# Kernel optimization log

Hardware: AMD Instinct MI355X
Metric: run time of the kernel (lower is better)

Reference implementation:

```python
import jax, jax.numpy as jnp
import numpy as np
from jax.ops import segment_sum, segment_max

N_NODES = 100000
N_EDGES = 1600000
IN_CH = 128
HIDDEN = 128
OUT_CH = 64
HEADS1 = 8


def _lin_params(key, din, dout, scale):
    kw, kb = jax.random.split(key)
    W = jax.random.normal(kw, (din, dout), jnp.float32) * scale
    b = jax.random.normal(kb, (dout,), jnp.float32) * 0.01
    return W, b


def setup_inputs() -> dict:
    key = jax.random.key(0)
    ks = jax.random.split(key, 10)
    x = jax.random.normal(ks[0], (N_NODES, IN_CH), jnp.float32)
    edge_index = jax.random.randint(ks[1], (2, N_EDGES), 0, N_NODES, jnp.int32)
    s1 = 1.0 / np.sqrt(IN_CH)
    Wq1, bq1 = _lin_params(ks[2], IN_CH, HIDDEN, s1)
    Wk1, bk1 = _lin_params(ks[3], IN_CH, HIDDEN, s1)
    Wv1, bv1 = _lin_params(ks[4], IN_CH, HIDDEN, s1)
    Ws1, bs1 = _lin_params(ks[5], IN_CH, HIDDEN, s1)
    s2 = 1.0 / np.sqrt(HIDDEN)
    Wq2, bq2 = _lin_params(ks[6], HIDDEN, OUT_CH, s2)
    Wk2, bk2 = _lin_params(ks[7], HIDDEN, OUT_CH, s2)
    Wv2, bv2 = _lin_params(ks[8], HIDDEN, OUT_CH, s2)
    Ws2, bs2 = _lin_params(ks[9], HIDDEN, OUT_CH, s2)
    return dict(x=x, edge_index=edge_index,
                Wq1=Wq1, bq1=bq1, Wk1=Wk1, bk1=bk1, Wv1=Wv1, bv1=bv1, Ws1=Ws1, bs1=bs1,
                Wq2=Wq2, bq2=bq2, Wk2=Wk2, bk2=bk2, Wv2=Wv2, bv2=bv2, Ws2=Ws2, bs2=bs2)


def transformer_conv(x, src, dst, Wq, bq, Wk, bk, Wv, bv, Ws, bs, heads, concat):
    # x: [N, Din]; src/dst: [E]; per-head dim C = Dout_total // heads
    N = x.shape[0]
    C = Wq.shape[1] // heads
    q = (x @ Wq + bq).reshape(N, heads, C)
    k = (x @ Wk + bk).reshape(N, heads, C)
    v = (x @ Wv + bv).reshape(N, heads, C)
    # edge-wise gather + dot-product attention logits: [E, H]
    alpha = jnp.einsum('ehc,ehc->eh', q[dst], k[src]) / np.sqrt(C)
    # softmax over incoming edges of each dst node (stable via segment max)
    m = segment_max(alpha, dst, num_segments=N)  # [N, H]
    ex = jnp.exp(alpha - jax.lax.stop_gradient(m)[dst])
    denom = segment_sum(ex, dst, num_segments=N)  # [N, H]
    alpha_n = ex / denom[dst]  # [E, H]
    out = segment_sum(v[src] * alpha_n[:, :, None], dst, num_segments=N)  # [N, H, C]
    skip = x @ Ws + bs  # root weight (PyG root_weight=True)
    if concat:
        out = out.reshape(N, heads * C) + skip
    else:
        out = out.mean(axis=1) + skip
    return out


def reference(x, edge_index,
              Wq1, bq1, Wk1, bk1, Wv1, bv1, Ws1, bs1,
              Wq2, bq2, Wk2, bk2, Wv2, bv2, Ws2, bs2):
    src, dst = edge_index[0], edge_index[1]
    h = transformer_conv(x, src, dst, Wq1, bq1, Wk1, bk1, Wv1, bv1, Ws1, bs1,
                         heads=HEADS1, concat=True)
    h = jax.nn.relu(h)  # dropout is identity in eval mode
    out = transformer_conv(h, src, dst, Wq2, bq2, Wk2, bk2, Wv2, bv2, Ws2, bs2,
                           heads=1, concat=False)
    return out
```

## Files before the change

### kernel.cpp

```cpp
#include <hip/hip_runtime.h>
#include <math.h>

#define NN 100000
#define NE 1600000
#define NB 391
#define BKSH 8
#define EPB 6250
#define CSTAGE 5120
#define NDEG 64
#define DTOT (NDEG * NB)

typedef __attribute__((ext_vector_type(8))) short bf16x8;
typedef __attribute__((ext_vector_type(4))) float f32x4;

__device__ __forceinline__ unsigned short f2bf(float x) {
  unsigned int u = __float_as_uint(x);
  u += 0x7fffu + ((u >> 16) & 1u);
  return (unsigned short)(u >> 16);
}
__device__ __forceinline__ float bf2f(unsigned short b) {
  return __uint_as_float(((unsigned int)b) << 16);
}
__device__ __forceinline__ void unpack8(uint4 u, float* f) {
  f[0] = __uint_as_float(u.x << 16); f[1] = __uint_as_float(u.x & 0xffff0000u);
  f[2] = __uint_as_float(u.y << 16); f[3] = __uint_as_float(u.y & 0xffff0000u);
  f[4] = __uint_as_float(u.z << 16); f[5] = __uint_as_float(u.z & 0xffff0000u);
  f[6] = __uint_as_float(u.w << 16); f[7] = __uint_as_float(u.w & 0xffff0000u);
}
__device__ __forceinline__ void split8(const float* f, bf16x8& h8, bf16x8& l8) {
  union { bf16x8 v; unsigned short s[8]; } H, L;
  #pragma unroll
  for (int j = 0; j < 8; ++j) {
    const unsigned short hh = f2bf(f[j]);
    H.s[j] = hh;
    L.s[j] = f2bf(f[j] - bf2f(hh));
  }
  h8 = H.v; l8 = L.v;
}
__device__ __forceinline__ void gl_lds16(const void* g, void* lds) {
  __builtin_amdgcn_global_load_lds(
      (const __attribute__((address_space(1))) unsigned int*)g,
      (__attribute__((address_space(3))) unsigned int*)lds, 16, 0, 0);
}

__global__ __launch_bounds__(256)
void bktcnt_k(const int* __restrict__ dst, int* __restrict__ gcnt) {
  __shared__ int cnt[NB];
  for (int i = threadIdx.x; i < NB; i += 256) cnt[i] = 0;
  __syncthreads();
  const int e0 = blockIdx.x * EPB;
  for (int e = e0 + threadIdx.x; e < e0 + EPB; e += 256)
    atomicAdd(&cnt[dst[e] >> BKSH], 1);
  __syncthreads();
  for (int i = threadIdx.x; i < NB; i += 256)
    if (cnt[i]) atomicAdd(&gcnt[i], cnt[i]);
}

__global__ void bktscan_k(const int* __restrict__ gcnt, int* __restrict__ base,
                          int* __restrict__ cursor) {
  __shared__ int sh[512];
  const int t = threadIdx.x;
  const int v = (t < NB) ? gcnt[t] : 0;
  sh[t] = v;
  __syncthreads();
  #pragma unroll
  for (int off = 1; off < 512; off <<= 1) {
    int nv = (t >= off) ? sh[t - off] : 0;
    __syncthreads();
    sh[t] += nv;
    __syncthreads();
  }
  const int excl = sh[t] - v;
  if (t < NB) { base[t] = excl; cursor[t] = excl; }
  if (t == NB - 1) base[NB] = excl + v;
}

__global__ __launch_bounds__(256)
void bktscat_k(const int* __restrict__ src, const int* __restrict__ dst,
               int* __restrict__ cursor, unsigned int* __restrict__ pairs) {
  __shared__ int cnt[NB];
  __shared__ int bbase[NB];
  for (int i = threadIdx.x; i < NB; i += 256) cnt[i] = 0;
  __syncthreads();
  const int e0 = blockIdx.x * EPB;
  for (int e = e0 + threadIdx.x; e < e0 + EPB; e += 256)
    atomicAdd(&cnt[dst[e] >> BKSH], 1);
  __syncthreads();
  for (int i = threadIdx.x; i < NB; i += 256) {
    bbase[i] = cnt[i] ? atomicAdd(&cursor[i], cnt[i]) : 0;
    cnt[i] = 0;
  }
  __syncthreads();
  for (int e = e0 + threadIdx.x; e < e0 + EPB; e += 256) {
    const int d = dst[e];
    const int b = d >> BKSH;
    const int loc = atomicAdd(&cnt[b], 1);
    pairs[bbase[b] + loc] = ((unsigned)src[e] << BKSH) | (unsigned)(d & 255);
  }
}

__global__ __launch_bounds__(256)
void bktcsr_k(const unsigned int* __restrict__ pairs, const int* __restrict__ base,
              int* __restrict__ rowp, int* __restrict__ cidx) {
  __shared__ int cnt[256];
  __shared__ int sums[256];
  __shared__ int stage[CSTAGE];
  const int b = blockIdx.x, t = threadIdx.x;
  const int p0 = base[b], p1 = base[b + 1], bs = p1 - p0;
  const int n0 = b << BKSH;
  const int nloc = (NN - n0 < 256) ? (NN - n0) : 256;
  cnt[t] = 0;
  __syncthreads();
  for (int i = p0 + t; i < p1; i += 256)
    atomicAdd(&cnt[pairs[i] & 255], 1);
  __syncthreads();
  const int v = cnt[t];
  sums[t] = v;
  __syncthreads();
  #pragma unroll
  for (int off = 1; off < 256; off <<= 1) {
    int nv = (t >= off) ? sums[t - off] : 0;
    __syncthreads();
    sums[t] += nv;
    __syncthreads();
  }
  const int myexcl = sums[t] - v;
  if (t < nloc) rowp[n0 + t] = p0 + myexcl;
  if (b == 0 && t == 0) rowp[NN] = base[NB];
  __syncthreads();
  cnt[t] = myexcl;
  __syncthreads();
  if (bs <= CSTAGE) {
    for (int i = p0 + t; i < p1; i += 256) {
      const unsigned pk = pairs[i];
      const int loc = atomicAdd(&cnt[pk & 255], 1);
      stage[loc] = (int)(pk >> BKSH);
    }
    __syncthreads();
    for (int i = t; i < bs; i += 256) cidx[p0 + i] = stage[i];
  } else {
    for (int i = p0 + t; i < p1; i += 256) {
      const unsigned pk = pairs[i];
      const int loc = atomicAdd(&cnt[pk & 255], 1);
      cidx[p0 + loc] = (int)(pk >> BKSH);
    }
  }
}

__global__ __launch_bounds__(256)
void dcnt_k(const int* __restrict__ rowp, int* __restrict__ gdcnt) {
  __shared__ int h[NDEG];
  const int t = threadIdx.x, b = blockIdx.x;
  if (t < NDEG) h[t] = 0;
  __syncthreads();
  const int n = b * 256 + t;
  if (n < NN) {
    int d = rowp[n + 1] - rowp[n];
    if (d > NDEG - 1) d = NDEG - 1;
    atomicAdd(&h[d], 1);
  }
  __syncthreads();
  if (t < NDEG) gdcnt[t * NB + b] = h[t];
}

__global__ __launch_bounds__(1024)
void dscan2_k(int* __restrict__ g) {
  __shared__ int part[1024];
  const int t = threadIdx.x;
  constexpr int PER = (DTOT + 1023) / 1024;
  int vals[PER];
  const int base = t * PER;
  int sum = 0;
  #pragma unroll
  for (int i = 0; i < PER; ++i) {
    const int idx = base + i;
    const int v = (idx < DTOT) ? g[idx] : 0;
    vals[i] = sum;
    sum += v;
  }
  part[t] = sum;
  __syncthreads();
  #pragma unroll
  for (int off = 1; off < 1024; off <<= 1) {
    int nv = (t >= off) ? part[t - off] : 0;
    __syncthreads();
    part[t] += nv;
    __syncthreads();
  }
  const int excl = part[t] - sum;
  #pragma unroll
  for (int i = 0; i < PER; ++i) {
    const int idx = base + i;
    if (idx < DTOT) g[idx] = excl + vals[i];
  }
}

__global__ __launch_bounds__(256)
void dperm2_k(const int* __restrict__ rowp, const int* __restrict__ gdcnt,
              int* __restrict__ perm) {
  __shared__ int lcur[NDEG];
  const int t = threadIdx.x, b = blockIdx.x;
  if (t < NDEG) lcur[t] = 0;
  __syncthreads();
  const int n = b * 256 + t;
  if (n < NN) {
    int d = rowp[n + 1] - rowp[n];
    if (d > NDEG - 1) d = NDEG - 1;
    const int r = atomicAdd(&lcur[d], 1);
    perm[gdcnt[d * NB + b] + r] = n;
  }
}

struct WConv { const float* src; unsigned short* hi; unsigned short* lo; int dout; };
struct WConv8 { WConv m[8]; };

__global__ void wconv_k(WConv8 a) {
  const WConv w = a.m[blockIdx.x];
  const int n = 128 * w.dout;
  for (int i = threadIdx.x; i < n; i += blockDim.x) {
    const int c = i >> 7, kk = i & 127;
    const float x = w.src[(size_t)kk * w.dout + c];
    const unsigned short h = f2bf(x);
    w.hi[i] = h;
    w.lo[i] = f2bf(x - bf2f(h));
  }
}

struct GMat { const unsigned short* wh; const unsigned short* wl;
              const float* bias; float* outf; unsigned short* outb; };
struct GArgs { GMat m[4]; };

template <int DOUT, bool PRESPLIT>
__global__ __launch_bounds__(256, 3)
void gemm4_mfma(const float* __restrict__ X,
                const unsigned short* __restrict__ Xh,
                const unsigned short* __restrict__ Xl,
                int nrows, GArgs ga) {
  constexpr int NCG = DOUT / 64;
  constexpr int NS = 4 * NCG * 2;
  __shared__ __align__(16) unsigned short Bs[2][8192];
  const int t = threadIdx.x;
  const int w = t >> 6, l = t & 63;
  const int lr = l & 15, lg = l >> 4;
  const int row0 = blockIdx.x * 128;

  bf16x8 ah[2][4], al[2][4];
  #pragma unroll
  for (int rf = 0; rf < 2; ++rf) {
    const int r = row0 + w * 32 + rf * 16 + lr;
    const bool ok = r < nrows;
    if constexpr (!PRESPLIT) {
      const float* xp = &X[(size_t)r * 128];
      #pragma unroll
      for (int ks = 0; ks < 4; ++ks) {
        float f[8];
        if (ok) {
          *(float4*)&f[0] = *(const float4*)&xp[ks * 32 + lg * 8];
          *(float4*)&f[4] = *(const float4*)&xp[ks * 32 + lg * 8 + 4];
        } else {
          #pragma unroll
          for (int j = 0; j < 8; ++j) f[j] = 0.f;
        }
        split8(f, ah[rf][ks], al[rf][ks]);
      }
    } else {
      #pragma unroll
      for (int ks = 0; ks < 4; ++ks) {
        if (ok) {
          ah[rf][ks] = *(const bf16x8*)&Xh[(size_t)r * 128 + ks * 32 + lg * 8];
          al[rf][ks] = *(const bf16x8*)&Xl[(size_t)r * 128 + ks * 32 + lg * 8];
        } else {
          union { bf16x8 v; unsigned short s[8]; } z;
          #pragma unroll
          for (int j = 0; j < 8; ++j) z.s[j] = 0;
          ah[rf][ks] = z.v; al[rf][ks] = z.v;
        }
      }
    }
  }

  auto stage = [&](int buf, int s) {
    const int m = s / (NCG * 2);
    const int rem = s - m * (NCG * 2);
    const int cg = rem >> 1, pl = rem & 1;
    const char* gb = (const char*)((pl ? ga.m[m].wl : ga.m[m].wh) + cg * 64 * 128);
    char* lb = (char*)&Bs[buf][0];
    #pragma unroll
    for (int i = 0; i < 4; ++i) {
      const int seg = (w * 4 + i) << 10;
      const int o = seg + l * 16;
      const int osw = o ^ (((o >> 8) & 7) << 4);
      gl_lds16(gb + osw, lb + seg);
    }
  };

  f32x4 acc[4][2];
  stage(0, 0);
  __syncthreads();
  int cur = 0;
  const int sw = (lr & 7) << 4;
  for (int s = 0; s < NS; ++s) {
    if (s + 1 < NS) stage(cur ^ 1, s + 1);
    const int m = s / (NCG * 2);
    const int rem = s - m * (NCG * 2);
    const int cg = rem >> 1, pl = rem & 1;
    const char* lbase = (const char*)&Bs[cur][0];
    if (pl == 0) {
      #pragma unroll
      for (int nf = 0; nf < 4; ++nf) {
        const char* lp = lbase + nf * 4096 + lr * 256;
        bf16x8 bq[4];
        #pragma unroll
        for (int ks = 0; ks < 4; ++ks)
          bq[ks] = *(const bf16x8*)(lp + (((ks * 64 + lg * 16) ^ sw)));
        f32x4 a0 = {0.f, 0.f, 0.f, 0.f}, a1 = a0;
        #pragma unroll
        for (int ks = 0; ks < 4; ++ks) {
          a0 = __builtin_amdgcn_mfma_f32_16x16x32_bf16(ah[0][ks], bq[ks], a0, 0, 0, 0);
          a1 = __builtin_amdgcn_mfma_f32_16x16x32_bf16(ah[1][ks], bq[ks], a1, 0, 0, 0);
        }
        #pragma unroll
        for (int ks = 0; ks < 4; ++ks) {
          a0 = __builtin_amdgcn_mfma_f32_16x16x32_bf16(al[0][ks], bq[ks], a0, 0, 0, 0);
          a1 = __builtin_amdgcn_mfma_f32_16x16x32_bf16(al[1][ks], bq[ks], a1, 0, 0, 0);
        }
        acc[nf][0] = a0; acc[nf][1] = a1;
      }
    } else {
      const GMat gm = ga.m[m];
      #pragma unroll
      for (int nf = 0; nf < 4; ++nf) {
        const char* lp = lbase + nf * 4096 + lr * 256;
        bf16x8 bq[4];
        #pragma unroll
        for (int ks = 0; ks < 4; ++ks)
          bq[ks] = *(const bf16x8*)(lp + (((ks * 64 + lg * 16) ^ sw)));
        f32x4 a0 = acc[nf][0], a1 = acc[nf][1];
        #pragma unroll
        for (int ks = 0; ks < 4; ++ks) {
          a0 = __builtin_amdgcn_mfma_f32_16x16x32_bf16(ah[0][ks], bq[ks], a0, 0, 0, 0);
          a1 = __builtin_amdgcn_mfma_f32_16x16x32_bf16(ah[1][ks], bq[ks], a1, 0, 0, 0);
        }
        const int col = cg * 64 + nf * 16 + lr;
        const float bb = gm.bias[col];
        #pragma unroll
        for (int j = 0; j < 4; ++j) {
          const int r0 = row0 + w * 32 + lg * 4 + j;
          const int r1 = r0 + 16;
          if (gm.outb) {
            if (r0 < nrows) gm.outb[(size_t)r0 * DOUT + col] = f2bf(a0[j] + bb);
            if (r1 < nrows) gm.outb[(size_t)r1 * DOUT + col] = f2bf(a1[j] + bb);
          } else {
            if (r0 < nrows) gm.outf[(size_t)r0 * DOUT + col] = a0[j] + bb;
            if (r1 < nrows) gm.outf[(size_t)r1 * DOUT + col] = a1[j] + bb;
          }
        }
      }
    }
    __syncthreads();
    cur ^= 1;
  }
}

__global__ __launch_bounds__(256)
void attn1_k(const unsigned short* __restrict__ q, const unsigned short* __restrict__ k,
             const unsigned short* __restrict__ v, const float* __restrict__ skip,
             const int* __restrict__ rowp, const int* __restrict__ cidx,
             const int* __restrict__ perm,
             unsigned short* __restrict__ hhi, unsigned short* __restrict__ hlo) {
  const int idx = blockIdx.x * 32 + (threadIdx.x >> 3);
  if (idx >= NN) return;
  const int node = perm[idx];
  const int cb = (threadIdx.x & 7) * 16;
  float qv[16];
  {
    uint4 q0 = *(const uint4*)&q[(size_t)node * 128 + cb];
    uint4 q1 = *(const uint4*)&q[(size_t)node * 128 + cb + 8];
    unpack8(q0, qv); unpack8(q1, qv + 8);
    #pragma unroll
    for (int c = 0; c < 16; ++c) qv[c] *= 0.25f;
  }
  float s = 0.f, acc[16];
  #pragma unroll
  for (int c = 0; c < 16; ++c) acc[c] = 0.f;
  const int e0 = rowp[node], e1 = rowp[node + 1];
  int e = e0;
  for (; e + 1 < e1; e += 2) {
    const int sa = cidx[e], sb = cidx[e + 1];
    const uint4 ka0 = *(const uint4*)&k[(size_t)sa * 128 + cb];
    const uint4 ka1 = *(const uint4*)&k[(size_t)sa * 128 + cb + 8];
    const uint4 kb0 = *(const uint4*)&k[(size_t)sb * 128 + cb];
    const uint4 kb1 = *(const uint4*)&k[(size_t)sb * 128 + cb + 8];
    const uint4 va0 = *(const uint4*)&v[(size_t)sa * 128 + cb];
    const uint4 va1 = *(const uint4*)&v[(size_t)sa * 128 + cb + 8];
    const uint4 vb0 = *(const uint4*)&v[(size_t)sb * 128 + cb];
    const uint4 vb1 = *(const uint4*)&v[(size_t)sb * 128 + cb + 8];
    float kva[16], kvb[16];
    unpack8(ka0, kva); unpack8(ka1, kva + 8);
    unpack8(kb0, kvb); unpack8(kb1, kvb + 8);
    float da = 0.f, db = 0.f;
    #pragma unroll
    for (int c = 0; c < 16; ++c) { da = fmaf(qv[c], kva[c], da); db = fmaf(qv[c], kvb[c], db); }
    const float pa = __expf(da), pb = __expf(db);
    s += pa + pb;
    float vva[16], vvb[16];
    unpack8(va0, vva); unpack8(va1, vva + 8);
    unpack8(vb0, vvb); unpack8(vb1, vvb + 8);
    #pragma unroll
    for (int c = 0; c < 16; ++c)
      acc[c] = fmaf(pb, vvb[c], fmaf(pa, vva[c], acc[c]));
  }
  if (e < e1) {
    const int sa = cidx[e];
    uint4 k0 = *(const uint4*)&k[(size_t)sa * 128 + cb];
    uint4 k1 = *(const uint4*)&k[(size_t)sa * 128 + cb + 8];
    float kv[16]; unpack8(k0, kv); unpack8(k1, kv + 8);
    float d = 0.f;
    #pragma unroll
    for (int c = 0; c < 16; ++c) d = fmaf(qv[c], kv[c], d);
    const float p = __expf(d);
    s += p;
    uint4 v0 = *(const uint4*)&v[(size_t)sa * 128 + cb];
    uint4 v1 = *(const uint4*)&v[(size_t)sa * 128 + cb + 8];
    float vv[16]; unpack8(v0, vv); unpack8(v1, vv + 8);
    #pragma unroll
    for (int c = 0; c < 16; ++c) acc[c] = fmaf(p, vv[c], acc[c]);
  }
  const float inv = (e1 > e0) ? 1.f / s : 0.f;
  float sk[16];
  {
    const float* sp = &skip[(size_t)node * 128 + cb];
    *(float4*)&sk[0]  = *(const float4*)&sp[0];
    *(float4*)&sk[4]  = *(const float4*)&sp[4];
    *(float4*)&sk[8]  = *(const float4*)&sp[8];
    *(float4*)&sk[12] = *(const float4*)&sp[12];
  }
  unsigned int hw[8], lw[8];
  #pragma unroll
  for (int c2 = 0; c2 < 8; ++c2) {
    const float oa = fmaxf(fmaf(acc[2 * c2], inv, sk[2 * c2]), 0.f);
    const float ob = fmaxf(fmaf(acc[2 * c2 + 1], inv, sk[2 * c2 + 1]), 0.f);
    const unsigned short ha = f2bf(oa), hb = f2bf(ob);
    hw[c2] = (unsigned)ha | ((unsigned)hb << 16);
    lw[c2] = (unsigned)f2bf(oa - bf2f(ha)) | ((unsigned)f2bf(ob - bf2f(hb)) << 16);
  }
  uint4* HH = (uint4*)&hhi[(size_t)node * 128 + cb];
  uint4* LL = (uint4*)&hlo[(size_t)node * 128 + cb];
  HH[0] = make_uint4(hw[0], hw[1], hw[2], hw[3]);
  HH[1] = make_uint4(hw[4], hw[5], hw[6], hw[7]);
  LL[0] = make_uint4(lw[0], lw[1], lw[2], lw[3]);
  LL[1] = make_uint4(lw[4], lw[5], lw[6], lw[7]);
}

__global__ __launch_bounds__(256)
void attn2_k(const unsigned short* __restrict__ q, const unsigned short* __restrict__ k,
             const unsigned short* __restrict__ v, const float* __restrict__ skip,
             const int* __restrict__ rowp, const int* __restrict__ cidx,
             const int* __restrict__ perm, float* __restrict__ out) {
  const int idx = blockIdx.x * 32 + (threadIdx.x >> 3);
  if (idx >= NN) return;
  const int node = perm[idx];
  const int cb = (threadIdx.x & 7) * 8;
  float qv[8];
  {
    uint4 q0 = *(const uint4*)&q[(size_t)node * 64 + cb];
    unpack8(q0, qv);
    #pragma unroll
    for (int c = 0; c < 8; ++c) qv[c] *= 0.125f;
  }
  float s = 0.f, acc[8];
  #pragma unroll
  for (int c = 0; c < 8; ++c) acc[c] = 0.f;
  const int e0 = rowp[node], e1 = rowp[node + 1];
  int e = e0;
  for (; e + 1 < e1; e += 2) {
    const int sa = cidx[e], sb = cidx[e + 1];
    const uint4 ka = *(const uint4*)&k[(size_t)sa * 64 + cb];
    const uint4 kb = *(const uint4*)&k[(size_t)sb * 64 + cb];
    const uint4 va = *(const uint4*)&v[(size_t)sa * 64 + cb];
    const uint4 vb = *(const uint4*)&v[(size_t)sb * 64 + cb];
    float kva[8], kvb[8];
    unpack8(ka, kva); unpack8(kb, kvb);
    float da = 0.f, db = 0.f;
    #pragma unroll
    for (int c = 0; c < 8; ++c) { da = fmaf(qv[c], kva[c], da); db = fmaf(qv[c], kvb[c], db); }
    da += __shfl_xor(da, 1); db += __shfl_xor(db, 1);
    da += __shfl_xor(da, 2); db += __shfl_xor(db, 2);
    da += __shfl_xor(da, 4); db += __shfl_xor(db, 4);
    const float pa = __expf(da), pb = __expf(db);
    s += pa + pb;
    float vva[8], vvb[8];
    unpack8(va, vva); unpack8(vb, vvb);
    #pragma unroll
    for (int c = 0; c < 8; ++c)
      acc[c] = fmaf(pb, vvb[c], fmaf(pa, vva[c], acc[c]));
  }
  if (e < e1) {
    const int sa = cidx[e];
    uint4 kk = *(const uint4*)&k[(size_t)sa * 64 + cb];
    float kv[8]; unpack8(kk, kv);
    float d = 0.f;
    #pragma unroll
    for (int c = 0; c < 8; ++c) d = fmaf(qv[c], kv[c], d);
    d += __shfl_xor(d, 1);
    d += __shfl_xor(d, 2);
    d += __shfl_xor(d, 4);
    const float p = __expf(d);
    s += p;
    uint4 vv4 = *(const uint4*)&v[(size_t)sa * 64 + cb];
    float vv[8]; unpack8(vv4, vv);
    #pragma unroll
    for (int c = 0; c < 8; ++c) acc[c] = fmaf(p, vv[c], acc[c]);
  }
  const float inv = (e1 > e0) ? 1.f / s : 0.f;
  const float* sp = &skip[(size_t)node * 64 + cb];
  float4 o0, o1;
  o0.x = fmaf(acc[0], inv, sp[0]); o0.y = fmaf(acc[1], inv, sp[1]);
  o0.z = fmaf(acc[2], inv, sp[2]); o0.w = fmaf(acc[3], inv, sp[3]);
  o1.x = fmaf(acc[4], inv, sp[4]); o1.y = fmaf(acc[5], inv, sp[5]);
  o1.z = fmaf(acc[6], inv, sp[6]); o1.w = fmaf(acc[7], inv, sp[7]);
  *(float4*)&out[(size_t)node * 64 + cb] = o0;
  *(float4*)&out[(size_t)node * 64 + cb + 4] = o1;
}

extern "C" void kernel_launch(void* const* d_in, const int* in_sizes, int n_in,
                              void* d_out, int out_size, void* d_ws, size_t ws_size,
                              hipStream_t stream) {
  const float* x = (const float*)d_in[0];
  const int* ei = (const int*)d_in[1];
  const int* esrc = ei;
  const int* edst = ei + NE;
  const float* Wf[8] = {(const float*)d_in[2],  (const float*)d_in[4],
                        (const float*)d_in[6],  (const float*)d_in[8],
                        (const float*)d_in[10], (const float*)d_in[12],
                        (const float*)d_in[14], (const float*)d_in[16]};
  const float* Bf[8] = {(const float*)d_in[3],  (const float*)d_in[5],
                        (const float*)d_in[7],  (const float*)d_in[9],
                        (const float*)d_in[11], (const float*)d_in[13],
                        (const float*)d_in[15], (const float*)d_in[17]};
  float* out = (float*)d_out;

  char* p = (char*)d_ws;
  auto alloc = [&](size_t b) { char* r = p; p += (b + 255) & ~(size_t)255; return r; };
  unsigned short* q1 = (unsigned short*)alloc((size_t)NN * 128 * 2);
  unsigned short* k1 = (unsigned short*)alloc((size_t)NN * 128 * 2);
  unsigned short* v1 = (unsigned short*)alloc((size_t)NN * 128 * 2);
  float*          sk1 = (float*)alloc((size_t)NN * 128 * 4);
  unsigned short* hh = (unsigned short*)alloc((size_t)NN * 128 * 2);
  unsigned short* hl = (unsigned short*)alloc((size_t)NN * 128 * 2);
  unsigned short* q2 = (unsigned short*)alloc((size_t)NN * 64 * 2);
  unsigned short* k2 = (unsigned short*)alloc((size_t)NN * 64 * 2);
  unsigned short* v2 = (unsigned short*)alloc((size_t)NN * 64 * 2);
  float*          sk2 = (float*)alloc((size_t)NN * 64 * 4);
  unsigned short* wh[8];
  unsigned short* wl[8];
  for (int i = 0; i < 8; ++i) {
    const int dout = (i < 4) ? 128 : 64;
    wh[i] = (unsigned short*)alloc((size_t)128 * dout * 2);
    wl[i] = (unsigned short*)alloc((size_t)128 * dout * 2);
  }
  int* rowp = (int*)alloc((size_t)(NN + 1) * 4);
  int* cidx = (int*)alloc((size_t)NE * 4);
  int* gcnt = (int*)alloc((size_t)NB * 4);
  int* base = (int*)alloc((size_t)(NB + 1) * 4);
  int* cursor = (int*)alloc((size_t)NB * 4);
  int* gdcnt = (int*)alloc((size_t)DTOT * 4);
  int* perm = (int*)alloc((size_t)NN * 4);
  unsigned int* pairs = (unsigned int*)hh;

  WConv8 wc;
  for (int i = 0; i < 8; ++i) wc.m[i] = {Wf[i], wh[i], wl[i], (i < 4) ? 128 : 64};
  wconv_k<<<8, 1024, 0, stream>>>(wc);

  hipMemsetAsync(gcnt, 0, NB * sizeof(int), stream);
  bktcnt_k<<<256, 256, 0, stream>>>(edst, gcnt);
  bktscan_k<<<1, 512, 0, stream>>>(gcnt, base, cursor);
  bktscat_k<<<256, 256, 0, stream>>>(esrc, edst, cursor, pairs);
  bktcsr_k<<<NB, 256, 0, stream>>>(pairs, base, rowp, cidx);

  dcnt_k<<<NB, 256, 0, stream>>>(rowp, gdcnt);
  dscan2_k<<<1, 1024, 0, stream>>>(gdcnt);
  dperm2_k<<<NB, 256, 0, stream>>>(rowp, gdcnt, perm);

  GArgs g1;
  g1.m[0] = {wh[0], wl[0], Bf[0], nullptr, q1};
  g1.m[1] = {wh[1], wl[1], Bf[1], nullptr, k1};
  g1.m[2] = {wh[2], wl[2], Bf[2], nullptr, v1};
  g1.m[3] = {wh[3], wl[3], Bf[3], sk1, nullptr};
  gemm4_mfma<128, false><<<(NN + 127) / 128, 256, 0, stream>>>(x, nullptr, nullptr, NN, g1);
  attn1_k<<<(NN + 31) / 32, 256, 0, stream>>>(q1, k1, v1, sk1, rowp, cidx, perm, hh, hl);

  GArgs g2;
  g2.m[0] = {wh[4], wl[4], Bf[4], nullptr, q2};
  g2.m[1] = {wh[5], wl[5], Bf[5], nullptr, k2};
  g2.m[2] = {wh[6], wl[6], Bf[6], nullptr, v2};
  g2.m[3] = {wh[7], wl[7], Bf[7], sk2, nullptr};
  gemm4_mfma<64, true><<<(NN + 127) / 128, 256, 0, stream>>>(nullptr, hh, hl, NN, g2);
  attn2_k<<<(NN + 31) / 32, 256, 0, stream>>>(q2, k2, v2, sk2, rowp, cidx, perm, out);
}
```

Measured before the change: 474.4 us.

## Use vmcnt-based partial waits in GEMM pipeline and unroll attention edge loops by four

The GEMM double-buffer loop swaps its full __syncthreads for inline s_waitcnt vmcnt(16) plus s_barrier. This lets the prefetch of the next stage stay in flight while only the current stage's LDS loads are awaited. Both attention kernels now gather four edges' K/V rows per iteration instead of two, giving more memory-level parallelism per thread at the cost of extra registers. The vmcnt count is hand-tuned to the number of loads issued per stage, so it could be wrong if the compiler reorders or adds memory operations.

```diff
diff --git a/kernel.cpp b/kernel.cpp
--- a/kernel.cpp
+++ b/kernel.cpp
@@ -42,6 +42,10 @@
       (const __attribute__((address_space(1))) unsigned int*)g,
       (__attribute__((address_space(3))) unsigned int*)lds, 16, 0, 0);
 }
+
+#define PIPE_WAIT16 asm volatile("s_waitcnt vmcnt(16)\n\ts_barrier" ::: "memory")
+#define PIPE_WAIT0  asm volatile("s_waitcnt vmcnt(0)\n\ts_barrier" ::: "memory")
+#define PIPE_BAR    asm volatile("s_barrier" ::: "memory")
 
 __global__ __launch_bounds__(256)
 void bktcnt_k(const int* __restrict__ dst, int* __restrict__ gcnt) {
@@ -296,11 +300,15 @@
 
   f32x4 acc[4][2];
   stage(0, 0);
-  __syncthreads();
   int cur = 0;
   const int sw = (lr & 7) << 4;
   for (int s = 0; s < NS; ++s) {
-    if (s + 1 < NS) stage(cur ^ 1, s + 1);
+    if (s + 1 < NS) {
+      stage(cur ^ 1, s + 1);
+      PIPE_WAIT16;
+    } else {
+      PIPE_WAIT0;
+    }
     const int m = s / (NCG * 2);
     const int rem = s - m * (NCG * 2);
     const int cg = rem >> 1, pl = rem & 1;
@@ -357,7 +365,7 @@
         }
       }
     }
-    __syncthreads();
+    if (s + 1 < NS) PIPE_BAR;
     cur ^= 1;
   }
 }
@@ -385,43 +393,50 @@
   for (int c = 0; c < 16; ++c) acc[c] = 0.f;
   const int e0 = rowp[node], e1 = rowp[node + 1];
   int e = e0;
-  for (; e + 1 < e1; e += 2) {
-    const int sa = cidx[e], sb = cidx[e + 1];
-    const uint4 ka0 = *(const uint4*)&k[(size_t)sa * 128 + cb];
-    const uint4 ka1 = *(const uint4*)&k[(size_t)sa * 128 + cb + 8];
-    const uint4 kb0 = *(const uint4*)&k[(size_t)sb * 128 + cb];
-    const uint4 kb1 = *(const uint4*)&k[(size_t)sb * 128 + cb + 8];
-    const uint4 va0 = *(const uint4*)&v[(size_t)sa * 128 + cb];
-    const uint4 va1 = *(const uint4*)&v[(size_t)sa * 128 + cb + 8];
-    const uint4 vb0 = *(const uint4*)&v[(size_t)sb * 128 + cb];
-    const uint4 vb1 = *(const uint4*)&v[(size_t)sb * 128 + cb + 8];
-    float kva[16], kvb[16];
-    unpack8(ka0, kva); unpack8(ka1, kva + 8);
-    unpack8(kb0, kvb); unpack8(kb1, kvb + 8);
-    float da = 0.f, db = 0.f;
-    #pragma unroll
-    for (int c = 0; c < 16; ++c) { da = fmaf(qv[c], kva[c], da); db = fmaf(qv[c], kvb[c], db); }
-    const float pa = __expf(da), pb = __expf(db);
-    s += pa + pb;
-    float vva[16], vvb[16];
-    unpack8(va0, vva); unpack8(va1, vva + 8);
-    unpack8(vb0, vvb); unpack8(vb1, vvb + 8);
-    #pragma unroll
-    for (int c = 0; c < 16; ++c)
-      acc[c] = fmaf(pb, vvb[c], fmaf(pa, vva[c], acc[c]));
-  }
-  if (e < e1) {
+  for (; e + 3 < e1; e += 4) {
+    int sidx[4];
+    #pragma unroll
+    for (int j = 0; j < 4; ++j) sidx[j] = cidx[e + j];
+    uint4 K[4][2], V[4][2];
+    #pragma unroll
+    for (int j = 0; j < 4; ++j) {
+      const size_t o = (size_t)sidx[j] * 128 + cb;
+      K[j][0] = *(const uint4*)&k[o];
+      K[j][1] = *(const uint4*)&k[o + 8];
+      V[j][0] = *(const uint4*)&v[o];
+      V[j][1] = *(const uint4*)&v[o + 8];
+    }
+    float pr[4];
+    #pragma unroll
+    for (int j = 0; j < 4; ++j) {
+      float kv[16];
+      unpack8(K[j][0], kv); unpack8(K[j][1], kv + 8);
+      float d = 0.f;
+      #pragma unroll
+      for (int c = 0; c < 16; ++c) d = fmaf(qv[c], kv[c], d);
+      pr[j] = __expf(d);
+      s += pr[j];
+    }
+    #pragma unroll
+    for (int j = 0; j < 4; ++j) {
+      float vv[16];
+      unpack8(V[j][0], vv); unpack8(V[j][1], vv + 8);
+      #pragma unroll
+      for (int c = 0; c < 16; ++c) acc[c] = fmaf(pr[j], vv[c], acc[c]);
+    }
+  }
+  for (; e < e1; ++e) {
     const int sa = cidx[e];
     uint4 k0 = *(const uint4*)&k[(size_t)sa * 128 + cb];
     uint4 k1 = *(const uint4*)&k[(size_t)sa * 128 + cb + 8];
+    uint4 v0 = *(const uint4*)&v[(size_t)sa * 128 + cb];
+    uint4 v1 = *(const uint4*)&v[(size_t)sa * 128 + cb + 8];
     float kv[16]; unpack8(k0, kv); unpack8(k1, kv + 8);
     float d = 0.f;
     #pragma unroll
     for (int c = 0; c < 16; ++c) d = fmaf(qv[c], kv[c], d);
     const float p = __expf(d);
     s += p;
-    uint4 v0 = *(const uint4*)&v[(size_t)sa * 128 + cb];
-    uint4 v1 = *(const uint4*)&v[(size_t)sa * 128 + cb + 8];
     float vv[16]; unpack8(v0, vv); unpack8(v1, vv + 8);
     #pragma unroll
     for (int c = 0; c < 16; ++c) acc[c] = fmaf(p, vv[c], acc[c]);
@@ -473,31 +488,45 @@
   for (int c = 0; c < 8; ++c) acc[c] = 0.f;
   const int e0 = rowp[node], e1 = rowp[node + 1];
   int e = e0;
-  for (; e + 1 < e1; e += 2) {
-    const int sa = cidx[e], sb = cidx[e + 1];
-    const uint4 ka = *(const uint4*)&k[(size_t)sa * 64 + cb];
-    const uint4 kb = *(const uint4*)&k[(size_t)sb * 64 + cb];
-    const uint4 va = *(const uint4*)&v[(size_t)sa * 64 + cb];
-    const uint4 vb = *(const uint4*)&v[(size_t)sb * 64 + cb];
-    float kva[8], kvb[8];
-    unpack8(ka, kva); unpack8(kb, kvb);
-    float da = 0.f, db = 0.f;
-    #pragma unroll
-    for (int c = 0; c < 8; ++c) { da = fmaf(qv[c], kva[c], da); db = fmaf(qv[c], kvb[c], db); }
-    da += __shfl_xor(da, 1); db += __shfl_xor(db, 1);
-    da += __shfl_xor(da, 2); db += __shfl_xor(db, 2);
-    da += __shfl_xor(da, 4); db += __shfl_xor(db, 4);
-    const float pa = __expf(da), pb = __expf(db);
-    s += pa + pb;
-    float vva[8], vvb[8];
-    unpack8(va, vva); unpack8(vb, vvb);
-    #pragma unroll
-    for (int c = 0; c < 8; ++c)
-      acc[c] = fmaf(pb, vvb[c], fmaf(pa, vva[c], acc[c]));
-  }
-  if (e < e1) {
+  for (; e + 3 < e1; e += 4) {
+    int sidx[4];
+    #pragma unroll
+    for (int j = 0; j < 4; ++j) sidx[j] = cidx[e + j];
+    uint4 K[4], V[4];
+    #pragma unroll
+    for (int j = 0; j < 4; ++j) {
+      const size_t o = (size_t)sidx[j] * 64 + cb;
+      K[j] = *(const uint4*)&k[o];
+      V[j] = *(const uint4*)&v[o];
+    }
+    float dd[4];
+    #pragma unroll
+    for (int j = 0; j < 4; ++j) {
+      float kv[8]; unpack8(K[j], kv);
+      float d = 0.f;
+      #pragma unroll
+      for (int c = 0; c < 8; ++c) d = fmaf(qv[c], kv[c], d);
+      dd[j] = d;
+    }
+    #pragma unroll
+    for (int j = 0; j < 4; ++j) {
+      dd[j] += __shfl_xor(dd[j], 1);
+      dd[j] += __shfl_xor(dd[j], 2);
+      dd[j] += __shfl_xor(dd[j], 4);
+    }
+    #pragma unroll
+    for (int j = 0; j < 4; ++j) {
+      const float p = __expf(dd[j]);
+      s += p;
+      float vv[8]; unpack8(V[j], vv);
+      #pragma unroll
+      for (int c = 0; c < 8; ++c) acc[c] = fmaf(p, vv[c], acc[c]);
+    }
+  }
+  for (; e < e1; ++e) {
     const int sa = cidx[e];
     uint4 kk = *(const uint4*)&k[(size_t)sa * 64 + cb];
+    uint4 vv4 = *(const uint4*)&v[(size_t)sa * 64 + cb];
     float kv[8]; unpack8(kk, kv);
     float d = 0.f;
     #pragma unroll
@@ -507,7 +536,6 @@
     d += __shfl_xor(d, 4);
     const float p = __expf(d);
     s += p;
-    uint4 vv4 = *(const uint4*)&v[(size_t)sa * 64 + cb];
     float vv[8]; unpack8(vv4, vv);
     #pragma unroll
     for (int c = 0; c < 8; ++c) acc[c] = fmaf(p, vv[c], acc[c]);
```

Measured after the change: 474.9 us. No clear change (+0.1%).
